# Kernel tuning notes

Measured on AMD Instinct MI355X. Metric: run time of the kernel, lower is better.

## Reference

```python
import jax, jax.numpy as jnp
import numpy as np

NUM_HEADS = 8

def _mha(x, in_w, in_b, out_w, out_b):
    # x: [B, L, E]; in_w: [3E, E]; out_w: [E, E]
    B, L, E = x.shape
    H = NUM_HEADS
    Dh = E // H
    qkv = x @ in_w.T + in_b                      # [B, L, 3E]
    q, k, v = jnp.split(qkv, 3, axis=-1)
    # [B, H, L, Dh]
    q = q.reshape(B, L, H, Dh).transpose(0, 2, 1, 3)
    k = k.reshape(B, L, H, Dh).transpose(0, 2, 1, 3)
    v = v.reshape(B, L, H, Dh).transpose(0, 2, 1, 3)
    scale = 1.0 / jnp.sqrt(jnp.asarray(Dh, dtype=x.dtype))
    scores = jnp.einsum('bhld,bhsd->bhls', q, k) * scale   # [B, H, L, S]
    attn = jax.nn.softmax(scores, axis=-1)
    ctx = jnp.einsum('bhls,bhsd->bhld', attn, v)           # [B, H, L, Dh]
    ctx = ctx.transpose(0, 2, 1, 3).reshape(B, L, E)
    out = ctx @ out_w.T + out_b                             # [B, L, E]
    # PyTorch default average_attn_weights=True: mean over heads -> [B, L, S]
    weights = attn.mean(axis=1)
    return out, weights

def setup_inputs() -> dict:
    key = jax.random.key(0)
    ks = jax.random.split(key, 5)
    B, L, E = 4, 2048, 1024
    s = 0.02
    return {
        'hidden_states': jax.random.normal(ks[0], (B, L, E), dtype=jnp.float32),
        'in_proj_w': jax.random.normal(ks[1], (3 * E, E), dtype=jnp.float32) * s,
        'in_proj_b': jnp.zeros((3 * E,), dtype=jnp.float32),
        'out_proj_w': jax.random.normal(ks[2], (E, E), dtype=jnp.float32) * s,
        'out_proj_b': jnp.zeros((E,), dtype=jnp.float32),
        'dep_proj_w': jax.random.normal(ks[3], (E, E), dtype=jnp.float32) * s,
        'dep_proj_b': jnp.zeros((E,), dtype=jnp.float32),
    }

def reference(hidden_states, in_proj_w, in_proj_b, out_proj_w, out_proj_b, dep_proj_w, dep_proj_b):
    enhanced, attn_weights = _mha(hidden_states, in_proj_w, in_proj_b, out_proj_w, out_proj_b)
    # dependency_scores: mean over query dim then key dim -> [B]
    dependency_scores = attn_weights.mean(axis=1).mean(axis=-1)
    enhanced = enhanced @ dep_proj_w.T + dep_proj_b
    return dependency_scores, enhanced
```

## Files before the change

kernel.cpp:

```cpp
#include <hip/hip_runtime.h>


typedef __attribute__((ext_vector_type(8))) short short8;
typedef __attribute__((ext_vector_type(4))) float float4v;
typedef __attribute__((ext_vector_type(4))) int int4v;
typedef __attribute__((ext_vector_type(2))) unsigned uint2v;

__device__ inline ushort f2bf(float f) {
  union { float f; unsigned u; } v; v.f = f;
  unsigned u = v.u;
  return (ushort)((u + 0x7FFFu + ((u >> 16) & 1u)) >> 16);
}
__device__ inline float bf2f(ushort h) {
  union { unsigned u; float f; } v; v.u = ((unsigned)h) << 16;
  return v.f;
}
__device__ inline unsigned pack2bf(float a, float b) {
  union { float f; unsigned u; } va, vb; va.f = a; vb.f = b;
  unsigned ua = va.u + 0x7FFFu + ((va.u >> 16) & 1u);
  unsigned ub = vb.u + 0x7FFFu + ((vb.u >> 16) & 1u);
  return __builtin_amdgcn_perm(ub, ua, 0x07060302);
}

__global__ __launch_bounds__(256)
void cvt_all(const float* __restrict__ X, const float* __restrict__ Wi,
             const float* __restrict__ Wd,
             ushort* __restrict__ Xb, ushort* __restrict__ Wib,
             ushort* __restrict__ Wdb) {
  size_t i = ((size_t)blockIdx.x * 256 + threadIdx.x) * 8;
  const float* src; ushort* dst;
  if (i < 8388608)        { src = X  + i;              dst = Xb  + i; }
  else if (i < 11534336)  { src = Wi + (i - 8388608);  dst = Wib + (i - 8388608); }
  else                    { src = Wd + (i - 11534336); dst = Wdb + (i - 11534336); }
  float4v a = *(const float4v*)(src);
  float4v b = *(const float4v*)(src + 4);
  ushort o[8];
  o[0] = f2bf(a.x); o[1] = f2bf(a.y); o[2] = f2bf(a.z); o[3] = f2bf(a.w);
  o[4] = f2bf(b.x); o[5] = f2bf(b.y); o[6] = f2bf(b.z); o[7] = f2bf(b.w);
  *(int4v*)dst = *(const int4v*)o;
}

__global__ __launch_bounds__(256)
void cvtT(const float* __restrict__ Wo, ushort* __restrict__ WoT) {
  __shared__ ushort Ts[64 * 72];
  const int t = threadIdx.x;
  const int ct = blockIdx.x * 64, rt = blockIdx.y * 64;
#pragma unroll
  for (int i = 0; i < 4; i++) {
    const int row = i * 16 + (t >> 4), col4 = (t & 15) * 4;
    float4v v = *(const float4v*)(Wo + (size_t)(rt + row) * 1024 + ct + col4);
    ushort o[4] = {f2bf(v.x), f2bf(v.y), f2bf(v.z), f2bf(v.w)};
    *(uint2v*)(Ts + row * 72 + col4) = *(const uint2v*)o;
  }
  __syncthreads();
#pragma unroll
  for (int it = 0; it < 2; it++) {
    const int c = it * 256 + t;
    const int oc = c >> 3, r8 = (c & 7) * 8;
    ushort o[8];
#pragma unroll
    for (int j = 0; j < 8; j++) o[j] = Ts[(r8 + j) * 72 + oc];
    *(int4v*)(WoT + (size_t)(ct + oc) * 1024 + rt + r8) = *(const int4v*)o;
  }
}

__global__ __launch_bounds__(64)
void bck(const float* __restrict__ Wd, const float* __restrict__ bo,
         const float* __restrict__ bd, float* __restrict__ bc,
         float* __restrict__ dep) {
  const int row = blockIdx.x, lane = threadIdx.x;
  float s = 0.f;
#pragma unroll
  for (int i = 0; i < 4; i++) {
    const int j = i * 256 + lane * 4;
    float4v w = *(const float4v*)(Wd + (size_t)row * 1024 + j);
    float4v b = *(const float4v*)(bo + j);
    s += w.x * b.x + w.y * b.y + w.z * b.z + w.w * b.w;
  }
#pragma unroll
  for (int off = 1; off <= 32; off <<= 1) s += __shfl_xor(s, off);
  if (lane == 0) bc[row] = s + bd[row];
  if (row < 4 && lane == 1) dep[row] = 1.0f / 2048.0f;
}

template <bool OUT_BF16>
__global__ __launch_bounds__(256, 2)
void gemm_bt(const ushort* __restrict__ A, const ushort* __restrict__ W,
             const float* __restrict__ bias, void* __restrict__ Cv,
             int M, int N, int K) {
  __shared__ ushort As[128 * 32];
  __shared__ ushort Bs[128 * 32];
  const int t = threadIdx.x;
  const int w = t >> 6;
  const int lane = t & 63;
  const int m16 = lane & 15, quad = lane >> 4;
  const int bx = blockIdx.x, by = blockIdx.y;
  const int warpRow = w >> 1, warpCol = w & 1;

  const int srow = t >> 2;
  const int scol = (t & 3) * 8;
  const ushort* Aptr = A + (size_t)(by * 128) * K;
  const ushort* Wptr = W + (size_t)(bx * 128) * K;

  float4v zero4 = {0.f, 0.f, 0.f, 0.f};
  float4v acc[4][4];
#pragma unroll
  for (int i = 0; i < 4; i++)
#pragma unroll
    for (int j = 0; j < 4; j++) acc[i][j] = zero4;

  for (int k0 = 0; k0 < K; k0 += 32) {
    __syncthreads();
#pragma unroll
    for (int r = 0; r < 2; r++) {
      const ushort* g = Aptr + (size_t)(r * 64 + srow) * K + (k0 + scol);
      __builtin_amdgcn_global_load_lds(
          (const __attribute__((address_space(1))) void*)g,
          (__attribute__((address_space(3))) void*)(As + r * 2048 + t * 8),
          16, 0, 0);
    }
#pragma unroll
    for (int r = 0; r < 2; r++) {
      const ushort* g = Wptr + (size_t)(r * 64 + srow) * K + (k0 + scol);
      __builtin_amdgcn_global_load_lds(
          (const __attribute__((address_space(1))) void*)g,
          (__attribute__((address_space(3))) void*)(Bs + r * 2048 + t * 8),
          16, 0, 0);
    }
    __syncthreads();

    short8 af[4], bf[4];
#pragma unroll
    for (int i = 0; i < 4; i++) {
      af[i] = *(const short8*)(As + (warpRow * 64 + i * 16 + m16) * 32 + quad * 8);
      bf[i] = *(const short8*)(Bs + (warpCol * 64 + i * 16 + m16) * 32 + quad * 8);
    }
#pragma unroll
    for (int i = 0; i < 4; i++)
#pragma unroll
      for (int j = 0; j < 4; j++)
        acc[i][j] = __builtin_amdgcn_mfma_f32_16x16x32_bf16(af[i], bf[j],
                                                            acc[i][j], 0, 0, 0);
  }

  const int crow_base = by * 128 + warpRow * 64;
  const int ccol_base = bx * 128 + warpCol * 64;
#pragma unroll
  for (int j = 0; j < 4; j++) {
    const int col = ccol_base + j * 16 + m16;
    const float bv = bias ? bias[col] : 0.0f;
#pragma unroll
    for (int i = 0; i < 4; i++) {
      const int row = crow_base + i * 16 + quad * 4;
#pragma unroll
      for (int r = 0; r < 4; r++) {
        const float v = acc[i][j][r] + bv;
        if constexpr (OUT_BF16)
          ((ushort*)Cv)[(size_t)(row + r) * N + col] = f2bf(v);
        else
          ((float*)Cv)[(size_t)(row + r) * N + col] = v;
      }
    }
  }
}

__global__ __launch_bounds__(256, 2)
void vtrans(const ushort* __restrict__ qkv, ushort* __restrict__ Vt) {
  __shared__ ushort Vs[64 * 136];
  const int t = threadIdx.x;
  const int st = blockIdx.x, h = blockIdx.y, b = blockIdx.z;
  const ushort* src = qkv + ((size_t)(b * 2048 + st * 64)) * 3072 + 2048 + h * 128;

#pragma unroll
  for (int it = 0; it < 4; it++) {
    const int c = it * 256 + t;
    const int row = c >> 4, col8 = (c & 15) * 8;
    int4v v = *(const int4v*)(src + (size_t)row * 3072 + col8);
    *(int4v*)(Vs + row * 136 + col8) = v;
  }
  __syncthreads();

  const int d = t >> 1, sh = (t & 1) * 32;
  unsigned pk[16];
#pragma unroll
  for (int k = 0; k < 16; k++) {
    unsigned lo = Vs[(sh + 2 * k) * 136 + d];
    unsigned hi = Vs[(sh + 2 * k + 1) * 136 + d];
    pk[k] = lo | (hi << 16);
  }
  ushort* dst = Vt + ((size_t)((b * 8 + h) * 128 + d)) * 2048 + st * 64 + sh;
#pragma unroll
  for (int m = 0; m < 8; m++) {
    const int pos4 = ((m & 3) << 1) | (m >> 2);
    uint2v o;
    o.x = pk[2 * m];
    o.y = pk[2 * m + 1];
    *(uint2v*)(dst + pos4 * 4) = o;
  }
}

__global__ __launch_bounds__(256, 2)
void attn(const ushort* __restrict__ qkv, const ushort* __restrict__ Vt,
          ushort* __restrict__ ctx) {
  __shared__ ushort Ks[2][64 * 128];
  __shared__ ushort Vsm[2][128 * 64];
  const int t = threadIdx.x, w = t >> 6, lane = t & 63;
  const int m16 = lane & 15, quad = lane >> 4;
  const int qt = blockIdx.x, h = blockIdx.y, b = blockIdx.z;
  const int E3 = 3072;
  const size_t bbase = (size_t)b * 2048;

  const ushort* Qg = qkv + (bbase + qt * 128 + w * 32) * E3 + h * 128;
  const ushort* Kg = qkv + bbase * E3 + 1024 + h * 128;
  const ushort* Vg = Vt + (size_t)((b * 8 + h) * 128) * 2048;

  auto stage = [&](int kt, int buf) {
#pragma unroll
    for (int it = 0; it < 4; it++) {
      const int c = it * 256 + t;
      const int row = c >> 4, cir = c & 15;
      const int j = (cir & 8) | ((cir ^ row) & 7);
      const ushort* g = Kg + (size_t)(kt * 64 + row) * E3 + j * 8;
      __builtin_amdgcn_global_load_lds(
          (const __attribute__((address_space(1))) void*)g,
          (__attribute__((address_space(3))) void*)(&Ks[buf][c * 8]), 16, 0, 0);
    }
#pragma unroll
    for (int it = 0; it < 4; it++) {
      const int c = it * 256 + t;
      const int d = c >> 3, cir = c & 7;
      const int j = cir ^ (d & 7);
      const ushort* g = Vg + (size_t)d * 2048 + kt * 64 + j * 8;
      __builtin_amdgcn_global_load_lds(
          (const __attribute__((address_space(1))) void*)g,
          (__attribute__((address_space(3))) void*)(&Vsm[buf][c * 8]), 16, 0, 0);
    }
  };

  stage(0, 0);

  const float c1 = 0.08838834764831845f * 1.4426950408889634f;
  short8 qf[2][4];
#pragma unroll
  for (int g = 0; g < 2; g++)
#pragma unroll
    for (int ks = 0; ks < 4; ks++) {
      short8 raw = *(const short8*)(Qg + (size_t)(g * 16 + m16) * E3 + ks * 32 + quad * 8);
      short8 s;
#pragma unroll
      for (int j = 0; j < 8; j++) s[j] = (short)f2bf(bf2f((ushort)raw[j]) * c1);
      qf[g][ks] = s;
    }

  int kslot[4];
#pragma unroll
  for (int ks = 0; ks < 4; ks++) {
    const int j = ks * 4 + quad;
    kslot[ks] = (j & 8) | ((j ^ m16) & 7);
  }

  float4v zero4 = {0.f, 0.f, 0.f, 0.f};
  float4v Oacc[2][8];
#pragma unroll
  for (int g = 0; g < 2; g++)
#pragma unroll
    for (int dt = 0; dt < 8; dt++) Oacc[g][dt] = zero4;
  float lsum[2] = {0.f, 0.f};

  for (int kt = 0; kt < 32; kt++) {
    const int cur = kt & 1;
    __syncthreads();
    if (kt < 31) stage(kt + 1, cur ^ 1);
    const ushort* Ksb = Ks[cur];
    const ushort* Vsb = Vsm[cur];

#pragma unroll
    for (int half = 0; half < 2; half++) {
      float4v st[2][2];
      st[0][0] = zero4; st[0][1] = zero4; st[1][0] = zero4; st[1][1] = zero4;
#pragma unroll
      for (int ks = 0; ks < 4; ks++) {
#pragma unroll
        for (int mt2 = 0; mt2 < 2; mt2++) {
          short8 kf = *(const short8*)(Ksb + ((half * 2 + mt2) * 16 + m16) * 128 +
                                       kslot[ks] * 8);
          st[0][mt2] = __builtin_amdgcn_mfma_f32_16x16x32_bf16(kf, qf[0][ks], st[0][mt2], 0, 0, 0);
          st[1][mt2] = __builtin_amdgcn_mfma_f32_16x16x32_bf16(kf, qf[1][ks], st[1][mt2], 0, 0, 0);
        }
      }
      short8 pfr[2];
#pragma unroll
      for (int g = 0; g < 2; g++) {
        unsigned pk[4];
#pragma unroll
        for (int mt2 = 0; mt2 < 2; mt2++) {
          float p0 = __builtin_exp2f(st[g][mt2][0]);
          float p1 = __builtin_exp2f(st[g][mt2][1]);
          float p2 = __builtin_exp2f(st[g][mt2][2]);
          float p3 = __builtin_exp2f(st[g][mt2][3]);
          lsum[g] += (p0 + p1) + (p2 + p3);
          pk[mt2 * 2]     = pack2bf(p0, p1);
          pk[mt2 * 2 + 1] = pack2bf(p2, p3);
        }
        union { int4v i; short8 s; } pf;
        pf.i.x = (int)pk[0];
        pf.i.y = (int)pk[1];
        pf.i.z = (int)pk[2];
        pf.i.w = (int)pk[3];
        pfr[g] = pf.s;
      }
#pragma unroll
      for (int dt = 0; dt < 8; dt++) {
        const int vslot = (half * 4 + quad) ^ (m16 & 7);
        short8 vf = *(const short8*)(Vsb + (dt * 16 + m16) * 64 + vslot * 8);
        Oacc[0][dt] = __builtin_amdgcn_mfma_f32_16x16x32_bf16(pfr[0], vf, Oacc[0][dt], 0, 0, 0);
        Oacc[1][dt] = __builtin_amdgcn_mfma_f32_16x16x32_bf16(pfr[1], vf, Oacc[1][dt], 0, 0, 0);
      }
    }
  }

#pragma unroll
  for (int g = 0; g < 2; g++) {
    float l = lsum[g];
    l += __shfl_xor(l, 16);
    l += __shfl_xor(l, 32);
    float* lf = (float*)(&Ks[0][w * 64]);
    lf[m16] = l;
    float linv[4];
#pragma unroll
    for (int r = 0; r < 4; r++) linv[r] = 1.0f / lf[quad * 4 + r];
#pragma unroll
    for (int r = 0; r < 4; r++) {
      const int row = qt * 128 + w * 32 + g * 16 + quad * 4 + r;
      ushort* crow = ctx + (bbase + row) * 1024 + h * 128;
#pragma unroll
      for (int dt = 0; dt < 8; dt++)
        crow[dt * 16 + m16] = f2bf(Oacc[g][dt][r] * linv[r]);
    }
  }
}

extern "C" void kernel_launch(void* const* d_in, const int* in_sizes, int n_in,
                              void* d_out, int out_size, void* d_ws, size_t ws_size,
                              hipStream_t stream) {
  const float* X  = (const float*)d_in[0];
  const float* Wi = (const float*)d_in[1];
  const float* bi = (const float*)d_in[2];
  const float* Wo = (const float*)d_in[3];
  const float* bo = (const float*)d_in[4];
  const float* Wd = (const float*)d_in[5];
  const float* bd = (const float*)d_in[6];
  float* out = (float*)d_out;

  ushort* p    = (ushort*)d_ws;
  ushort* Xb   = p; p += (size_t)8192 * 1024;
  ushort* Wib  = p; p += (size_t)3072 * 1024;
  ushort* WoTb = p; p += (size_t)1024 * 1024;
  ushort* Wdb  = p; p += (size_t)1024 * 1024;
  ushort* qkv  = p; p += (size_t)8192 * 3072;
  ushort* Vt   = p; p += (size_t)4096 * 2048;
  float*  bc   = (float*)p;
  ushort* ctx  = Xb;
  ushort* Wcb  = Wib;

  cvt_all<<<6144, 256, 0, stream>>>(X, Wi, Wd, Xb, Wib, Wdb);
  cvtT<<<dim3(16, 16), 256, 0, stream>>>(Wo, WoTb);
  bck<<<1024, 64, 0, stream>>>(Wd, bo, bd, bc, out);
  gemm_bt<true><<<dim3(24, 64), 256, 0, stream>>>(Xb, Wib, bi, qkv, 8192, 3072, 1024);
  gemm_bt<true><<<dim3(8, 8), 256, 0, stream>>>(Wdb, WoTb, nullptr, Wcb, 1024, 1024, 1024);
  vtrans<<<dim3(32, 8, 4), 256, 0, stream>>>(qkv, Vt);
  attn<<<dim3(16, 8, 4), 256, 0, stream>>>(qkv, Vt, ctx);
  gemm_bt<false><<<dim3(8, 64), 256, 0, stream>>>(ctx, Wcb, bc, out + 4, 8192, 1024, 1024);
}
```

Baseline: 336.5 us.

## Fuse V transpose into QKV GEMM epilogue and merge weight-combine GEMM launch

The QKV projection GEMM now writes the V columns straight into the transposed Vt layout from its epilogue, which removes the separate vtrans kernel and its extra read and write of V. The small Wd·Wo combine GEMM is folded into the same launch as extra blocks when the workspace is large enough, and it gets its own buffer so it no longer aliases Wib. The attention kernel uses the hardware v_cvt_pk_bf16_f32 instruction for bf16 packing and raises wave priority around its MFMA sections with s_setprio. The trade-offs are strided partial stores in the V epilogue and a workspace-size-dependent code path.

```diff
diff --git a/kernel.cpp b/kernel.cpp
--- a/kernel.cpp
+++ b/kernel.cpp
@@ -15,11 +15,10 @@
   union { unsigned u; float f; } v; v.u = ((unsigned)h) << 16;
   return v.f;
 }
-__device__ inline unsigned pack2bf(float a, float b) {
-  union { float f; unsigned u; } va, vb; va.f = a; vb.f = b;
-  unsigned ua = va.u + 0x7FFFu + ((va.u >> 16) & 1u);
-  unsigned ub = vb.u + 0x7FFFu + ((vb.u >> 16) & 1u);
-  return __builtin_amdgcn_perm(ub, ua, 0x07060302);
+__device__ inline unsigned cvtpk(float lo, float hi) {
+  unsigned r;
+  asm("v_cvt_pk_bf16_f32 %0, %1, %2" : "=v"(r) : "v"(lo), "v"(hi));
+  return r;
 }
 
 __global__ __launch_bounds__(256)
@@ -165,37 +164,119 @@
 }
 
 __global__ __launch_bounds__(256, 2)
-void vtrans(const ushort* __restrict__ qkv, ushort* __restrict__ Vt) {
-  __shared__ ushort Vs[64 * 136];
+void gemm_qkv(const ushort* __restrict__ Xb, const ushort* __restrict__ Wib,
+              const float* __restrict__ bi, ushort* __restrict__ qkv,
+              ushort* __restrict__ Vt,
+              const ushort* __restrict__ A2, const ushort* __restrict__ W2,
+              ushort* __restrict__ C2) {
+  __shared__ ushort As[128 * 32];
+  __shared__ ushort Bs[128 * 32];
   const int t = threadIdx.x;
-  const int st = blockIdx.x, h = blockIdx.y, b = blockIdx.z;
-  const ushort* src = qkv + ((size_t)(b * 2048 + st * 64)) * 3072 + 2048 + h * 128;
-
-#pragma unroll
-  for (int it = 0; it < 4; it++) {
-    const int c = it * 256 + t;
-    const int row = c >> 4, col8 = (c & 15) * 8;
-    int4v v = *(const int4v*)(src + (size_t)row * 3072 + col8);
-    *(int4v*)(Vs + row * 136 + col8) = v;
-  }
-  __syncthreads();
-
-  const int d = t >> 1, sh = (t & 1) * 32;
-  unsigned pk[16];
-#pragma unroll
-  for (int k = 0; k < 16; k++) {
-    unsigned lo = Vs[(sh + 2 * k) * 136 + d];
-    unsigned hi = Vs[(sh + 2 * k + 1) * 136 + d];
-    pk[k] = lo | (hi << 16);
-  }
-  ushort* dst = Vt + ((size_t)((b * 8 + h) * 128 + d)) * 2048 + st * 64 + sh;
-#pragma unroll
-  for (int m = 0; m < 8; m++) {
-    const int pos4 = ((m & 3) << 1) | (m >> 2);
-    uint2v o;
-    o.x = pk[2 * m];
-    o.y = pk[2 * m + 1];
-    *(uint2v*)(dst + pos4 * 4) = o;
+  const int w = t >> 6;
+  const int lane = t & 63;
+  const int m16 = lane & 15, quad = lane >> 4;
+  const int bid = blockIdx.x;
+  const bool second = bid >= 1536;
+  int bx, by;
+  const ushort *A, *W;
+  if (!second) { bx = bid % 24; by = bid / 24; A = Xb; W = Wib; }
+  else { const int b2 = bid - 1536; bx = b2 & 7; by = b2 >> 3; A = A2; W = W2; }
+  const int warpRow = w >> 1, warpCol = w & 1;
+  const int K = 1024;
+
+  const int srow = t >> 2;
+  const int scol = (t & 3) * 8;
+  const ushort* Aptr = A + (size_t)(by * 128) * K;
+  const ushort* Wptr = W + (size_t)(bx * 128) * K;
+
+  float4v zero4 = {0.f, 0.f, 0.f, 0.f};
+  float4v acc[4][4];
+#pragma unroll
+  for (int i = 0; i < 4; i++)
+#pragma unroll
+    for (int j = 0; j < 4; j++) acc[i][j] = zero4;
+
+  for (int k0 = 0; k0 < K; k0 += 32) {
+    __syncthreads();
+#pragma unroll
+    for (int r = 0; r < 2; r++) {
+      const ushort* g = Aptr + (size_t)(r * 64 + srow) * K + (k0 + scol);
+      __builtin_amdgcn_global_load_lds(
+          (const __attribute__((address_space(1))) void*)g,
+          (__attribute__((address_space(3))) void*)(As + r * 2048 + t * 8),
+          16, 0, 0);
+    }
+#pragma unroll
+    for (int r = 0; r < 2; r++) {
+      const ushort* g = Wptr + (size_t)(r * 64 + srow) * K + (k0 + scol);
+      __builtin_amdgcn_global_load_lds(
+          (const __attribute__((address_space(1))) void*)g,
+          (__attribute__((address_space(3))) void*)(Bs + r * 2048 + t * 8),
+          16, 0, 0);
+    }
+    __syncthreads();
+
+    short8 af[4], bf[4];
+#pragma unroll
+    for (int i = 0; i < 4; i++) {
+      af[i] = *(const short8*)(As + (warpRow * 64 + i * 16 + m16) * 32 + quad * 8);
+      bf[i] = *(const short8*)(Bs + (warpCol * 64 + i * 16 + m16) * 32 + quad * 8);
+    }
+#pragma unroll
+    for (int i = 0; i < 4; i++)
+#pragma unroll
+      for (int j = 0; j < 4; j++)
+        acc[i][j] = __builtin_amdgcn_mfma_f32_16x16x32_bf16(af[i], bf[j],
+                                                            acc[i][j], 0, 0, 0);
+  }
+
+  const int crow_base = by * 128 + warpRow * 64;
+  const int ccol_base = bx * 128 + warpCol * 64;
+
+  if (second) {
+#pragma unroll
+    for (int j = 0; j < 4; j++) {
+      const int col = ccol_base + j * 16 + m16;
+#pragma unroll
+      for (int i = 0; i < 4; i++) {
+        const int row = crow_base + i * 16 + quad * 4;
+#pragma unroll
+        for (int r = 0; r < 4; r++)
+          C2[(size_t)(row + r) * 1024 + col] = f2bf(acc[i][j][r]);
+      }
+    }
+  } else if (bx < 16) {
+#pragma unroll
+    for (int j = 0; j < 4; j++) {
+      const int col = ccol_base + j * 16 + m16;
+      const float bv = bi[col];
+#pragma unroll
+      for (int i = 0; i < 4; i++) {
+        const int row = crow_base + i * 16 + quad * 4;
+#pragma unroll
+        for (int r = 0; r < 4; r++)
+          qkv[(size_t)(row + r) * 3072 + col] = f2bf(acc[i][j][r] + bv);
+      }
+    }
+  } else {
+    const int b = by >> 4;
+#pragma unroll
+    for (int j = 0; j < 4; j++) {
+      const int col = ccol_base + j * 16 + m16;
+      const float bv = bi[col];
+      const int vcol = col - 2048;
+      const int h = vcol >> 7, d = vcol & 127;
+      ushort* vrow = Vt + (size_t)((b * 8 + h) * 128 + d) * 2048;
+#pragma unroll
+      for (int i = 0; i < 4; i++) {
+        const int pos = ((by & 15) << 7) + warpRow * 64 + ((i >> 1) << 5) +
+                        (2 * quad + (i & 1)) * 4;
+        uint2v o;
+        o.x = cvtpk(acc[i][j][0] + bv, acc[i][j][1] + bv);
+        o.y = cvtpk(acc[i][j][2] + bv, acc[i][j][3] + bv);
+        *(uint2v*)(vrow + pos) = o;
+      }
+    }
   }
 }
 
@@ -278,6 +359,7 @@
     for (int half = 0; half < 2; half++) {
       float4v st[2][2];
       st[0][0] = zero4; st[0][1] = zero4; st[1][0] = zero4; st[1][1] = zero4;
+      __builtin_amdgcn_s_setprio(1);
 #pragma unroll
       for (int ks = 0; ks < 4; ks++) {
 #pragma unroll
@@ -288,6 +370,7 @@
           st[1][mt2] = __builtin_amdgcn_mfma_f32_16x16x32_bf16(kf, qf[1][ks], st[1][mt2], 0, 0, 0);
         }
       }
+      __builtin_amdgcn_s_setprio(0);
       short8 pfr[2];
 #pragma unroll
       for (int g = 0; g < 2; g++) {
@@ -299,8 +382,8 @@
           float p2 = __builtin_exp2f(st[g][mt2][2]);
           float p3 = __builtin_exp2f(st[g][mt2][3]);
           lsum[g] += (p0 + p1) + (p2 + p3);
-          pk[mt2 * 2]     = pack2bf(p0, p1);
-          pk[mt2 * 2 + 1] = pack2bf(p2, p3);
+          pk[mt2 * 2]     = cvtpk(p0, p1);
+          pk[mt2 * 2 + 1] = cvtpk(p2, p3);
         }
         union { int4v i; short8 s; } pf;
         pf.i.x = (int)pk[0];
@@ -309,6 +392,7 @@
         pf.i.w = (int)pk[3];
         pfr[g] = pf.s;
       }
+      __builtin_amdgcn_s_setprio(1);
 #pragma unroll
       for (int dt = 0; dt < 8; dt++) {
         const int vslot = (half * 4 + quad) ^ (m16 & 7);
@@ -316,6 +400,7 @@
         Oacc[0][dt] = __builtin_amdgcn_mfma_f32_16x16x32_bf16(pfr[0], vf, Oacc[0][dt], 0, 0, 0);
         Oacc[1][dt] = __builtin_amdgcn_mfma_f32_16x16x32_bf16(pfr[1], vf, Oacc[1][dt], 0, 0, 0);
       }
+      __builtin_amdgcn_s_setprio(0);
     }
   }
 
@@ -359,16 +444,24 @@
   ushort* Wdb  = p; p += (size_t)1024 * 1024;
   ushort* qkv  = p; p += (size_t)8192 * 3072;
   ushort* Vt   = p; p += (size_t)4096 * 2048;
-  float*  bc   = (float*)p;
-  ushort* ctx  = Xb;
-  ushort* Wcb  = Wib;
+  float*  bc   = (float*)p; p += 2048;
+  ushort* WcbSep = p; p += (size_t)1024 * 1024;
+  const size_t need_merged = (size_t)((char*)p - (char*)d_ws);
+  const bool merged = ws_size >= need_merged;
+
+  ushort* ctx = Xb;
+  ushort* Wcb = merged ? WcbSep : Wib;
 
   cvt_all<<<6144, 256, 0, stream>>>(X, Wi, Wd, Xb, Wib, Wdb);
   cvtT<<<dim3(16, 16), 256, 0, stream>>>(Wo, WoTb);
   bck<<<1024, 64, 0, stream>>>(Wd, bo, bd, bc, out);
-  gemm_bt<true><<<dim3(24, 64), 256, 0, stream>>>(Xb, Wib, bi, qkv, 8192, 3072, 1024);
-  gemm_bt<true><<<dim3(8, 8), 256, 0, stream>>>(Wdb, WoTb, nullptr, Wcb, 1024, 1024, 1024);
-  vtrans<<<dim3(32, 8, 4), 256, 0, stream>>>(qkv, Vt);
+  if (merged) {
+    gemm_qkv<<<1600, 256, 0, stream>>>(Xb, Wib, bi, qkv, Vt, Wdb, WoTb, Wcb);
+  } else {
+    gemm_qkv<<<1536, 256, 0, stream>>>(Xb, Wib, bi, qkv, Vt, Wdb, WoTb, nullptr);
+    gemm_bt<true><<<dim3(8, 8), 256, 0, stream>>>(Wdb, WoTb, nullptr, Wcb,
+                                                  1024, 1024, 1024);
+  }
   attn<<<dim3(16, 8, 4), 256, 0, stream>>>(qkv, Vt, ctx);
   gemm_bt<false><<<dim3(8, 64), 256, 0, stream>>>(ctx, Wcb, bc, out + 4, 8192, 1024, 1024);
 }
```

After: 300.2 us. -10.8%, faster.
